# Performance work log

Hardware: AMD Instinct MI355X
Metric: run time of the kernel (lower is better)

The kernel has to match this reference:

```python
import jax, jax.numpy as jnp
import numpy as np

B, S, D, H = 2, 2048, 1024, 16
DH = D // H  # 64


def setup_inputs() -> dict:
    key = jax.random.key(0)
    ks = jax.random.split(key, 9)
    def rn(k, shape, scale=1.0):
        return jax.random.normal(k, shape, dtype=jnp.float32) * scale
    w_scale = 1.0 / np.sqrt(D)
    return {
        "queries": rn(ks[0], (B, S, D)),
        "keys": rn(ks[1], (B, S, D)),
        "values": rn(ks[2], (B, S, D)),
        "Wq": rn(ks[3], (D, D), w_scale),
        "bq": rn(ks[4], (D,), w_scale),
        "Wk": rn(ks[5], (D, D), w_scale),
        "bk": rn(ks[6], (D,), w_scale),
        "Wv": rn(ks[7], (D, D), w_scale),
        "bv": rn(ks[8], (D,), w_scale),
    }


def _split_heads(x):
    # torch: cat(split(x, DH, dim=-1), dim=0) -> index (h*B + b); equivalent to
    # [B,S,H,DH] -> [H,B,S,DH]
    bsz, slen, _ = x.shape
    return x.reshape(bsz, slen, H, DH).transpose(2, 0, 1, 3)


def reference(queries, keys, values, Wq, bq, Wk, bk, Wv, bv):
    # Linear projections (W stored so that y = x @ W + b)
    Q = queries @ Wq + bq
    K = keys @ Wk + bk
    V = values @ Wv + bv

    Qh = _split_heads(Q)  # [H,B,S,DH]
    Kh = _split_heads(K)
    Vh = _split_heads(V)

    scale = 1.0 / jnp.sqrt(jnp.asarray(DH, dtype=Qh.dtype))
    scores = jnp.einsum("hbqd,hbkd->hbqk", Qh, Kh) * scale  # [H,B,S,S]
    attn = jax.nn.softmax(scores, axis=-1)  # dropout_rate=0 -> identity
    out = jnp.einsum("hbqk,hbkd->hbqd", attn, Vh)  # [H,B,S,DH]

    # torch: cat(split(out, B, dim=0), dim=2) -> [B,S,H*DH] with head h in slice h
    out = out.transpose(1, 2, 0, 3).reshape(queries.shape[0], queries.shape[1], D)
    return out + queries  # residual; NOTE: W_O is defined but unused in the original forward
```

## Files before the change

### kernel.cpp

```cpp
#include <hip/hip_runtime.h>
#include <hip/hip_bf16.h>
#include <math.h>

#define BB 2
#define SS 2048
#define DD 1024
#define HH 16
#define DHH 64
#define MM (BB * SS)

typedef float f32x4 __attribute__((ext_vector_type(4)));
typedef float f32x16 __attribute__((ext_vector_type(16)));
typedef __bf16 bf16x8 __attribute__((ext_vector_type(8)));
typedef unsigned int u32x2 __attribute__((ext_vector_type(2)));

#define N_QKV ((size_t)MM * DD)
#define N_W   ((size_t)DD * DD)

__device__ unsigned short g_X [3][N_QKV];
__device__ unsigned short g_Q [N_QKV];
__device__ unsigned short g_K [N_QKV];
__device__ unsigned short g_Vt[N_QKV];
__device__ unsigned short g_Wt[3][N_W];

__device__ __forceinline__ unsigned short f2bu(float f) {
    unsigned u = __float_as_uint(f);
    unsigned r = u + 0x7FFFu + ((u >> 16) & 1u);
    return (unsigned short)(r >> 16);
}

union FragU { uint4 u; bf16x8 v; unsigned short s[8]; };
static __device__ __forceinline__ bf16x8 ldfrag(const unsigned short* p) {
    FragU f; f.u = *(const uint4*)p; return f.v;
}

static __device__ __forceinline__ unsigned pkbf(float a, float b) {
    union { __bf16 h[2]; unsigned u; } w;
    w.h[0] = (__bf16)a; w.h[1] = (__bf16)b;
    return w.u;
}

static __device__ __forceinline__ float fexp2(float x) {
#if __has_builtin(__builtin_amdgcn_exp2f)
    return __builtin_amdgcn_exp2f(x);
#else
    return __expf(x * 0.6931471805599453f);
#endif
}

static __device__ __forceinline__ void plswap(unsigned &a, unsigned &b) {
#if __has_builtin(__builtin_amdgcn_permlane32_swap)
    u32x2 r = __builtin_amdgcn_permlane32_swap((int)a, (int)b, false, false);
    a = r[0]; b = r[1];
#else
    const bool hi = (threadIdx.x & 63) >= 32;
    unsigned x = hi ? a : b;
    unsigned y = (unsigned)__shfl_xor((int)x, 32);
    unsigned na = hi ? y : a;
    unsigned nb = hi ? b : y;
    a = na; b = nb;
#endif
}

__global__ __launch_bounds__(256) void cvt3(
        const float* __restrict__ x0, const float* __restrict__ x1,
        const float* __restrict__ x2, unsigned short* __restrict__ X)
{
    const float* src = blockIdx.y == 0 ? x0 : (blockIdx.y == 1 ? x1 : x2);
    unsigned short* dst = X + (size_t)blockIdx.y * N_QKV;
    const size_t i = ((size_t)blockIdx.x * 256 + threadIdx.x) * 4;
    const float4 v = *(const float4*)(src + i);
    ushort4 s;
    s.x = f2bu(v.x); s.y = f2bu(v.y); s.z = f2bu(v.z); s.w = f2bu(v.w);
    *(ushort4*)(dst + i) = s;
}

__global__ __launch_bounds__(256) void transpose_w3(
        const float* __restrict__ W0, const float* __restrict__ W1,
        const float* __restrict__ W2, unsigned short* __restrict__ Wt3)
{
    const float* W = blockIdx.z == 0 ? W0 : (blockIdx.z == 1 ? W1 : W2);
    unsigned short* Wt = Wt3 + (size_t)blockIdx.z * N_W;
    __shared__ float Ts[64][65];
    const int t = threadIdx.x;
    const int k0 = blockIdx.y * 64, n0 = blockIdx.x * 64;
#pragma unroll
    for (int i = 0; i < 16; ++i) {
        const int f = t + 256 * i, r = f >> 6, c = f & 63;
        Ts[r][c] = W[(size_t)(k0 + r) * DD + n0 + c];
    }
    __syncthreads();
#pragma unroll
    for (int i = 0; i < 16; ++i) {
        const int f = t + 256 * i, r = f >> 6, c = f & 63;
        Wt[(size_t)(n0 + r) * DD + k0 + c] = f2bu(Ts[c][r]);
    }
}

__global__ __launch_bounds__(256) void proj3(
        const unsigned short* __restrict__ X, const unsigned short* __restrict__ Wt3,
        const float* __restrict__ bq, const float* __restrict__ bk,
        const float* __restrict__ bv,
        unsigned short* __restrict__ Qp, unsigned short* __restrict__ Kp,
        unsigned short* __restrict__ Vtp)
{
    const int z = blockIdx.z;
    const unsigned short* xb = X   + (size_t)z * N_QKV;
    const unsigned short* Wt = Wt3 + (size_t)z * N_W;
    const float* bias = z == 0 ? bq : (z == 1 ? bk : bv);
    const float scale = z == 0 ? 0.18033688011112042f : 1.0f;

    __shared__ unsigned short As[128][72];
    __shared__ unsigned short Bs[128][72];
    const int t = threadIdx.x, lane = t & 63, w = t >> 6;
    const int q = lane >> 4, li = lane & 15;
    const int wm = (w >> 1) * 64, wn = (w & 1) * 64;
    const int m0 = blockIdx.y * 128, n0 = blockIdx.x * 128;
    const int rs = t >> 3, cs = (t & 7) * 8;

    f32x4 acc[4][4];
#pragma unroll
    for (int mt = 0; mt < 4; ++mt)
#pragma unroll
        for (int nt = 0; nt < 4; ++nt) acc[mt][nt] = (f32x4)0.f;

    uint4 pa0, pa1, pa2, pa3, pb0, pb1, pb2, pb3;
#define PROJ_LD(kk) \
    pa0 = *(const uint4*)(xb + (size_t)(m0 + rs      ) * DD + (kk) + cs); \
    pa1 = *(const uint4*)(xb + (size_t)(m0 + rs + 32 ) * DD + (kk) + cs); \
    pa2 = *(const uint4*)(xb + (size_t)(m0 + rs + 64 ) * DD + (kk) + cs); \
    pa3 = *(const uint4*)(xb + (size_t)(m0 + rs + 96 ) * DD + (kk) + cs); \
    pb0 = *(const uint4*)(Wt + (size_t)(n0 + rs      ) * DD + (kk) + cs); \
    pb1 = *(const uint4*)(Wt + (size_t)(n0 + rs + 32 ) * DD + (kk) + cs); \
    pb2 = *(const uint4*)(Wt + (size_t)(n0 + rs + 64 ) * DD + (kk) + cs); \
    pb3 = *(const uint4*)(Wt + (size_t)(n0 + rs + 96 ) * DD + (kk) + cs);

    PROJ_LD(0)

    for (int kk = 0; kk < DD; kk += 64) {
        *(uint4*)&As[rs     ][cs] = pa0;
        *(uint4*)&As[rs + 32][cs] = pa1;
        *(uint4*)&As[rs + 64][cs] = pa2;
        *(uint4*)&As[rs + 96][cs] = pa3;
        *(uint4*)&Bs[rs     ][cs] = pb0;
        *(uint4*)&Bs[rs + 32][cs] = pb1;
        *(uint4*)&Bs[rs + 64][cs] = pb2;
        *(uint4*)&Bs[rs + 96][cs] = pb3;
        __syncthreads();
        if (kk + 64 < DD) { PROJ_LD(kk + 64) }
#pragma unroll
        for (int ks = 0; ks < 64; ks += 32) {
            bf16x8 a[4], b[4];
#pragma unroll
            for (int mt = 0; mt < 4; ++mt) a[mt] = ldfrag(&As[wm + mt * 16 + li][ks + q * 8]);
#pragma unroll
            for (int nt = 0; nt < 4; ++nt) b[nt] = ldfrag(&Bs[wn + nt * 16 + li][ks + q * 8]);
#pragma unroll
            for (int mt = 0; mt < 4; ++mt)
#pragma unroll
                for (int nt = 0; nt < 4; ++nt)
                    acc[mt][nt] = __builtin_amdgcn_mfma_f32_16x16x32_bf16(
                        a[mt], b[nt], acc[mt][nt], 0, 0, 0);
        }
        __syncthreads();
    }
#undef PROJ_LD

    float bvv[4];
#pragma unroll
    for (int nt = 0; nt < 4; ++nt) bvv[nt] = bias[n0 + wn + nt * 16 + li];

    if (z < 2) {
        unsigned short* out = z == 0 ? Qp : Kp;
#pragma unroll
        for (int mt = 0; mt < 4; ++mt)
#pragma unroll
            for (int nt = 0; nt < 4; ++nt)
#pragma unroll
                for (int reg = 0; reg < 4; ++reg) {
                    const int m = m0 + wm + mt * 16 + q * 4 + reg;
                    out[(size_t)m * DD + n0 + wn + nt * 16 + li] =
                        f2bu((acc[mt][nt][reg] + bvv[nt]) * scale);
                }
    } else {
        const int b = m0 >> 11;
        const int h = (n0 + wn) >> 6;
#pragma unroll
        for (int mt = 0; mt < 4; ++mt)
#pragma unroll
            for (int nt = 0; nt < 4; ++nt) {
                const int s = (m0 & (SS - 1)) + wm + mt * 16 + q * 4;
                const int dh = nt * 16 + li;
                ushort4 sv;
                sv.x = f2bu(acc[mt][nt][0] + bvv[nt]);
                sv.y = f2bu(acc[mt][nt][1] + bvv[nt]);
                sv.z = f2bu(acc[mt][nt][2] + bvv[nt]);
                sv.w = f2bu(acc[mt][nt][3] + bvv[nt]);
                *(ushort4*)(Vtp + ((size_t)((b * HH + h) * DHH + dh)) * SS + s) = sv;
            }
    }
}

__global__ __launch_bounds__(256) void attn6(
        const unsigned short* __restrict__ Qg, const unsigned short* __restrict__ Kg,
        const unsigned short* __restrict__ Vtg,
        const float* __restrict__ queries, float* __restrict__ outp)
{
    __shared__ unsigned short Kb[2][64][64];
    __shared__ unsigned short Vb[2][64][64];
    __shared__ float invL[4][32];

    const int t = threadIdx.x, lane = t & 63, w = t >> 6;
    const int col = lane & 31;
    const int hi  = lane >> 5;
    const int qt = blockIdx.x, h = blockIdx.y, b = blockIdx.z;

    const int sr = t >> 3;
    const int sc = t & 7;

    const unsigned short* Kbase = Kg  + (size_t)(b * SS) * DD + h * DHH;
    const unsigned short* Vbase = Vtg + ((size_t)((b * HH + h) * DHH)) * SS;

    bf16x8 qa[4];
    {
        const unsigned short* qp =
            Qg + (size_t)(b * SS + qt * 128 + w * 32 + col) * DD + h * DHH + hi * 8;
#pragma unroll
        for (int i = 0; i < 4; ++i) qa[i] = ldfrag(qp + i * 16);
    }

    f32x16 o0 = (f32x16)0.f, o1 = (f32x16)0.f;
    float lsum = 0.f;
    const int xr = col & 7;

    uint4 k0, k1, v0, v1;
#define LD_TILE(s0) \
    k0 = *(const uint4*)(Kbase + (size_t)((s0) + sr     ) * DD + sc * 8); \
    k1 = *(const uint4*)(Kbase + (size_t)((s0) + sr + 32) * DD + sc * 8); \
    v0 = *(const uint4*)(Vbase + (size_t)(sr     ) * SS + (s0) + sc * 8); \
    v1 = *(const uint4*)(Vbase + (size_t)(sr + 32) * SS + (s0) + sc * 8);

#define ST_TILE(buf) \
    *(uint4*)&Kb[buf][sr     ][(sc ^ (sr & 7)) * 8] = k0; \
    *(uint4*)&Kb[buf][sr + 32][(sc ^ (sr & 7)) * 8] = k1; \
    *(uint4*)&Vb[buf][sr     ][(sc ^ (sr & 7)) * 8] = v0; \
    *(uint4*)&Vb[buf][sr + 32][(sc ^ (sr & 7)) * 8] = v1;

    LD_TILE(0)
    ST_TILE(0)
    __syncthreads();

    const int NT = SS / 64;
#pragma unroll 2
    for (int kt = 0; kt < NT; ++kt) {
        const int cur = kt & 1;
        if (kt + 1 < NT) { LD_TILE((kt + 1) * 64) }

        f32x16 st0 = (f32x16)0.f, st1 = (f32x16)0.f;
#pragma unroll
        for (int i = 0; i < 4; ++i) {
            const int slot = ((i * 2 + hi) ^ xr) * 8;
            bf16x8 ka0 = ldfrag(&Kb[cur][col     ][slot]);
            bf16x8 ka1 = ldfrag(&Kb[cur][col + 32][slot]);
            st0 = __builtin_amdgcn_mfma_f32_32x32x16_bf16(ka0, qa[i], st0, 0, 0, 0);
            st1 = __builtin_amdgcn_mfma_f32_32x32x16_bf16(ka1, qa[i], st1, 0, 0, 0);
        }

        unsigned pkw[4][4];
        {
            float pe0[16], pe1[16];
#pragma unroll
            for (int r = 0; r < 16; ++r) { pe0[r] = fexp2(st0[r]); }
#pragma unroll
            for (int r = 0; r < 16; ++r) { pe1[r] = fexp2(st1[r]); }
            float ls = 0.f;
#pragma unroll
            for (int r = 0; r < 16; ++r) ls += pe0[r] + pe1[r];
            lsum += ls;
#pragma unroll
            for (int s = 0; s < 2; ++s) {
                pkw[s][0]     = pkbf(pe0[8 * s + 0], pe0[8 * s + 1]);
                pkw[s][1]     = pkbf(pe0[8 * s + 2], pe0[8 * s + 3]);
                pkw[s][2]     = pkbf(pe0[8 * s + 4], pe0[8 * s + 5]);
                pkw[s][3]     = pkbf(pe0[8 * s + 6], pe0[8 * s + 7]);
                pkw[2 + s][0] = pkbf(pe1[8 * s + 0], pe1[8 * s + 1]);
                pkw[2 + s][1] = pkbf(pe1[8 * s + 2], pe1[8 * s + 3]);
                pkw[2 + s][2] = pkbf(pe1[8 * s + 4], pe1[8 * s + 5]);
                pkw[2 + s][3] = pkbf(pe1[8 * s + 6], pe1[8 * s + 7]);
            }
        }

        if (kt + 1 < NT) { ST_TILE(cur ^ 1) }

#pragma unroll
        for (int c = 0; c < 4; ++c) {
            unsigned a0 = pkw[c][0], b0 = pkw[c][2];
            unsigned a1 = pkw[c][1], b1 = pkw[c][3];
            plswap(a0, b0);
            plswap(a1, b1);
            FragU pf;
            pf.u.x = a0; pf.u.y = a1; pf.u.z = b0; pf.u.w = b1;

            const int vs = ((c * 2 + hi) ^ xr) * 8;
            bf16x8 vb0 = ldfrag(&Vb[cur][col     ][vs]);
            bf16x8 vb1 = ldfrag(&Vb[cur][col + 32][vs]);
            o0 = __builtin_amdgcn_mfma_f32_32x32x16_bf16(pf.v, vb0, o0, 0, 0, 0);
            o1 = __builtin_amdgcn_mfma_f32_32x32x16_bf16(pf.v, vb1, o1, 0, 0, 0);
        }
        __syncthreads();
    }
#undef LD_TILE
#undef ST_TILE

    const float lt = lsum + __shfl_xor(lsum, 32);
    if (lane < 32) invL[w][lane] = 1.f / lt;
    __syncthreads();

    const size_t gbase = (size_t)(b * SS + qt * 128 + w * 32) * DD + h * DHH + col;
#pragma unroll
    for (int reg = 0; reg < 16; ++reg) {
        const int rl = (reg & 3) + 8 * (reg >> 2) + 4 * hi;
        const float inv = invL[w][rl];
        const size_t g = gbase + (size_t)rl * DD;
        outp[g]      = o0[reg] * inv + queries[g];
        outp[g + 32] = o1[reg] * inv + queries[g + 32];
    }
}

extern "C" void kernel_launch(void* const* d_in, const int* in_sizes, int n_in,
                              void* d_out, int out_size, void* d_ws, size_t ws_size,
                              hipStream_t stream) {
    const float* queries = (const float*)d_in[0];
    const float* keys    = (const float*)d_in[1];
    const float* values  = (const float*)d_in[2];
    const float* Wq      = (const float*)d_in[3];
    const float* bq      = (const float*)d_in[4];
    const float* Wk      = (const float*)d_in[5];
    const float* bk      = (const float*)d_in[6];
    const float* Wv      = (const float*)d_in[7];
    const float* bv      = (const float*)d_in[8];
    float* outp = (float*)d_out;

    const size_t need = (6 * N_QKV + 3 * N_W) * sizeof(unsigned short);
    unsigned short *Xp, *Qp, *Kp, *Vtp, *Wtp;
    if (ws_size >= need) {
        Xp  = (unsigned short*)d_ws;
        Qp  = Xp + 3 * N_QKV;
        Kp  = Qp + N_QKV;
        Vtp = Kp + N_QKV;
        Wtp = Vtp + N_QKV;
    } else {
        hipGetSymbolAddress((void**)&Xp,  HIP_SYMBOL(g_X));
        hipGetSymbolAddress((void**)&Qp,  HIP_SYMBOL(g_Q));
        hipGetSymbolAddress((void**)&Kp,  HIP_SYMBOL(g_K));
        hipGetSymbolAddress((void**)&Vtp, HIP_SYMBOL(g_Vt));
        hipGetSymbolAddress((void**)&Wtp, HIP_SYMBOL(g_Wt));
    }

    const dim3 bp(256);
    cvt3<<<dim3(MM * DD / 1024, 3), bp, 0, stream>>>(queries, keys, values, Xp);
    transpose_w3<<<dim3(16, 16, 3), bp, 0, stream>>>(Wq, Wk, Wv, Wtp);
    proj3<<<dim3(8, 32, 3), bp, 0, stream>>>(Xp, Wtp, bq, bk, bv, Qp, Kp, Vtp);
    attn6<<<dim3(SS / 128, HH, BB), bp, 0, stream>>>(Qp, Kp, Vtp, queries, outp);
}
```

Before: 205.9 us.

## Split attention KV sequence across two wave groups per block and merge partials

The attention kernel now launches 512 threads per block. Two groups of four waves each handle half of the key/value sequence, each with its own double-buffered LDS tiles. After the loop, group 1 writes its partial output accumulators and row sums into shared memory, and group 0 combines them, normalizes, and adds the residual. This doubles the waves available per query tile to hide latency, at the cost of more LDS per block, a reduction step, and possibly lower block occupancy. The fallback exp2 and permlane paths are switched to inline asm, and the row-sum accumulation is split into four partial sums.

```diff
diff --git a/kernel.cpp b/kernel.cpp
--- a/kernel.cpp
+++ b/kernel.cpp
@@ -44,7 +44,9 @@
 #if __has_builtin(__builtin_amdgcn_exp2f)
     return __builtin_amdgcn_exp2f(x);
 #else
-    return __expf(x * 0.6931471805599453f);
+    float r;
+    asm("v_exp_f32 %0, %1" : "=v"(r) : "v"(x));
+    return r;
 #endif
 }
 
@@ -53,12 +55,7 @@
     u32x2 r = __builtin_amdgcn_permlane32_swap((int)a, (int)b, false, false);
     a = r[0]; b = r[1];
 #else
-    const bool hi = (threadIdx.x & 63) >= 32;
-    unsigned x = hi ? a : b;
-    unsigned y = (unsigned)__shfl_xor((int)x, 32);
-    unsigned na = hi ? y : a;
-    unsigned nb = hi ? b : y;
-    a = na; b = nb;
+    asm volatile("v_permlane32_swap_b32 %0, %1" : "+v"(a), "+v"(b));
 #endif
 }
 
@@ -201,22 +198,27 @@
     }
 }
 
-__global__ __launch_bounds__(256) void attn6(
+__global__ __launch_bounds__(512, 4) void attn7(
         const unsigned short* __restrict__ Qg, const unsigned short* __restrict__ Kg,
         const unsigned short* __restrict__ Vtg,
         const float* __restrict__ queries, float* __restrict__ outp)
 {
-    __shared__ unsigned short Kb[2][64][64];
-    __shared__ unsigned short Vb[2][64][64];
-    __shared__ float invL[4][32];
-
-    const int t = threadIdx.x, lane = t & 63, w = t >> 6;
+    __shared__ unsigned short KVb[2][2][2][64][64];
+    __shared__ float Lp[2][4][32];
+
+    const int t = threadIdx.x, lane = t & 63;
+    const int g  = t >> 8;
+    const int wg = (t >> 6) & 3;
     const int col = lane & 31;
     const int hi  = lane >> 5;
     const int qt = blockIdx.x, h = blockIdx.y, b = blockIdx.z;
 
-    const int sr = t >> 3;
-    const int sc = t & 7;
+    const int tg = t & 255;
+    const int sr = tg >> 3;
+    const int sc = tg & 7;
+
+    unsigned short (*Kb)[64][64] = KVb[g][0];
+    unsigned short (*Vb)[64][64] = KVb[g][1];
 
     const unsigned short* Kbase = Kg  + (size_t)(b * SS) * DD + h * DHH;
     const unsigned short* Vbase = Vtg + ((size_t)((b * HH + h) * DHH)) * SS;
@@ -224,7 +226,7 @@
     bf16x8 qa[4];
     {
         const unsigned short* qp =
-            Qg + (size_t)(b * SS + qt * 128 + w * 32 + col) * DD + h * DHH + hi * 8;
+            Qg + (size_t)(b * SS + qt * 128 + wg * 32 + col) * DD + h * DHH + hi * 8;
 #pragma unroll
         for (int i = 0; i < 4; ++i) qa[i] = ldfrag(qp + i * 16);
     }
@@ -232,6 +234,7 @@
     f32x16 o0 = (f32x16)0.f, o1 = (f32x16)0.f;
     float lsum = 0.f;
     const int xr = col & 7;
+    const int kvofs = g << 10;
 
     uint4 k0, k1, v0, v1;
 #define LD_TILE(s0) \
@@ -246,15 +249,15 @@
     *(uint4*)&Vb[buf][sr     ][(sc ^ (sr & 7)) * 8] = v0; \
     *(uint4*)&Vb[buf][sr + 32][(sc ^ (sr & 7)) * 8] = v1;
 
-    LD_TILE(0)
+    LD_TILE(kvofs)
     ST_TILE(0)
     __syncthreads();
 
-    const int NT = SS / 64;
+    const int NT = 16;
 #pragma unroll 2
     for (int kt = 0; kt < NT; ++kt) {
         const int cur = kt & 1;
-        if (kt + 1 < NT) { LD_TILE((kt + 1) * 64) }
+        if (kt + 1 < NT) { LD_TILE(kvofs + (kt + 1) * 64) }
 
         f32x16 st0 = (f32x16)0.f, st1 = (f32x16)0.f;
 #pragma unroll
@@ -273,10 +276,15 @@
             for (int r = 0; r < 16; ++r) { pe0[r] = fexp2(st0[r]); }
 #pragma unroll
             for (int r = 0; r < 16; ++r) { pe1[r] = fexp2(st1[r]); }
-            float ls = 0.f;
-#pragma unroll
-            for (int r = 0; r < 16; ++r) ls += pe0[r] + pe1[r];
-            lsum += ls;
+            float s4[4] = {0.f, 0.f, 0.f, 0.f};
+#pragma unroll
+            for (int r = 0; r < 16; r += 4) {
+                s4[0] += pe0[r] + pe1[r];
+                s4[1] += pe0[r + 1] + pe1[r + 1];
+                s4[2] += pe0[r + 2] + pe1[r + 2];
+                s4[3] += pe0[r + 3] + pe1[r + 3];
+            }
+            lsum += (s4[0] + s4[1]) + (s4[2] + s4[3]);
 #pragma unroll
             for (int s = 0; s < 2; ++s) {
                 pkw[s][0]     = pkbf(pe0[8 * s + 0], pe0[8 * s + 1]);
@@ -313,17 +321,28 @@
 #undef ST_TILE
 
     const float lt = lsum + __shfl_xor(lsum, 32);
-    if (lane < 32) invL[w][lane] = 1.f / lt;
+    float* Ob = (float*)KVb;
+    const int obase = wg * 64 + lane;
+    if (g == 1) {
+#pragma unroll
+        for (int r = 0; r < 16; ++r) {
+            Ob[r * 256 + obase]        = o0[r];
+            Ob[(16 + r) * 256 + obase] = o1[r];
+        }
+    }
+    if (lane < 32) Lp[g][wg][lane] = lt;
     __syncthreads();
 
-    const size_t gbase = (size_t)(b * SS + qt * 128 + w * 32) * DD + h * DHH + col;
-#pragma unroll
-    for (int reg = 0; reg < 16; ++reg) {
-        const int rl = (reg & 3) + 8 * (reg >> 2) + 4 * hi;
-        const float inv = invL[w][rl];
-        const size_t g = gbase + (size_t)rl * DD;
-        outp[g]      = o0[reg] * inv + queries[g];
-        outp[g + 32] = o1[reg] * inv + queries[g + 32];
+    if (g == 0) {
+        const size_t gbase = (size_t)(b * SS + qt * 128 + wg * 32) * DD + h * DHH + col;
+#pragma unroll
+        for (int reg = 0; reg < 16; ++reg) {
+            const int rl = (reg & 3) + 8 * (reg >> 2) + 4 * hi;
+            const float li = 1.f / (Lp[0][wg][rl] + Lp[1][wg][rl]);
+            const size_t gaddr = gbase + (size_t)rl * DD;
+            outp[gaddr]      = (o0[reg] + Ob[reg * 256 + obase]) * li + queries[gaddr];
+            outp[gaddr + 32] = (o1[reg] + Ob[(16 + reg) * 256 + obase]) * li + queries[gaddr + 32];
+        }
     }
 }
 
@@ -361,5 +380,5 @@
     cvt3<<<dim3(MM * DD / 1024, 3), bp, 0, stream>>>(queries, keys, values, Xp);
     transpose_w3<<<dim3(16, 16, 3), bp, 0, stream>>>(Wq, Wk, Wv, Wtp);
     proj3<<<dim3(8, 32, 3), bp, 0, stream>>>(Xp, Wtp, bq, bk, bv, Qp, Kp, Vtp);
-    attn6<<<dim3(SS / 128, HH, BB), bp, 0, stream>>>(Qp, Kp, Vtp, queries, outp);
-}
+    attn7<<<dim3(SS / 128, HH, BB), dim3(512), 0, stream>>>(Qp, Kp, Vtp, queries, outp);
+}
```

Result: slower. 246.7 us (+19.8%).
